# Kernel tuning notes

Hardware: AMD Instinct MI355X
Metric: run time of the kernel (lower is better)

Reference implementation:

```python
import jax, jax.numpy as jnp
import numpy as np

N_QUBITS = 14
LATENT = 14
DEPTH = 4
BATCH = 256
DIM = 1 << N_QUBITS  # 16384 amplitudes

# PennyLane convention: wire 0 is the most-significant bit of the flat state index.
_idx = np.arange(DIM)
_bits = (_idx[None, :] >> (N_QUBITS - 1 - np.arange(N_QUBITS)[:, None])) & 1  # [n_qubits, DIM]
_parity = np.sum(_bits[:-1] * _bits[1:], axis=0) % 2  # adjacent-pair CZ chain parity
CZ_SIGNS = jnp.asarray(1.0 - 2.0 * _parity, dtype=jnp.complex64)  # [DIM]
Z_SIGNS = jnp.asarray(1 - 2 * _bits[:LATENT], dtype=jnp.float32)  # [LATENT, DIM]


def _rx(t):
    c = jnp.cos(0.5 * t) + 0j
    s = -1j * jnp.sin(0.5 * t)
    m = jnp.stack([jnp.stack([c, s], -1), jnp.stack([s, c], -1)], -2)
    return m.astype(jnp.complex64)


def _ry(t):
    c = jnp.cos(0.5 * t)
    s = jnp.sin(0.5 * t)
    m = jnp.stack([jnp.stack([c, -s], -1), jnp.stack([s, c], -1)], -2)
    return m.astype(jnp.complex64)


def _rz(t):
    e = jnp.exp(-0.5j * t.astype(jnp.complex64))
    z = jnp.zeros_like(e)
    m = jnp.stack([jnp.stack([e, z], -1), jnp.stack([z, jnp.conj(e)], -1)], -2)
    return m.astype(jnp.complex64)


def _apply_1q(state, mat, wire):
    # state: [B, DIM]; mat: [2,2] (shared) or [B,2,2] (per-sample)
    B = state.shape[0]
    left = 1 << wire
    right = 1 << (N_QUBITS - wire - 1)
    st = state.reshape(B, left, 2, right)
    if mat.ndim == 3:
        st = jnp.einsum('bij,bajc->baic', mat, st)
    else:
        st = jnp.einsum('ij,bajc->baic', mat, st)
    return st.reshape(B, DIM)


def setup_inputs() -> dict:
    key = jax.random.key(0)
    k1, k2, k3, k4 = jax.random.split(key, 4)
    conditioning = jax.random.normal(k1, (BATCH, LATENT), dtype=jnp.float32)
    lim = 1.0 / np.sqrt(LATENT)
    W_enc = jax.random.uniform(k2, (N_QUBITS, LATENT), jnp.float32, -lim, lim)
    b_enc = jax.random.uniform(k3, (N_QUBITS,), jnp.float32, -lim, lim)
    # TorchLayer default init: U(0, 2*pi)
    weights = jax.random.uniform(k4, (DEPTH, N_QUBITS, 3), jnp.float32, 0.0, 2.0 * np.pi)
    return {"conditioning": conditioning, "W_enc": W_enc, "b_enc": b_enc, "weights": weights}


def reference(conditioning, W_enc, b_enc, weights):
    # encode: Linear + SiLU -> per-wire rotation angles [B, n_qubits]
    emb = conditioning @ W_enc.T + b_enc
    emb = emb * jax.nn.sigmoid(emb)
    B = emb.shape[0]

    state = jnp.zeros((B, DIM), jnp.complex64).at[:, 0].set(1.0)

    # angle encoding: RX(v) then RY(v) on each wire (per-sample gates)
    for w in range(N_QUBITS):
        v = emb[:, w]
        U = jnp.einsum('bij,bjk->bik', _ry(v), _rx(v))  # [B,2,2]
        state = _apply_1q(state, U, w)

    # variational layers: RZ, RX, RY per wire (shared gates), then CZ chain
    for d in range(DEPTH):
        for w in range(N_QUBITS):
            p = weights[d, w]
            U = _ry(p[2]) @ _rx(p[1]) @ _rz(p[0])  # [2,2]
            state = _apply_1q(state, U, w)
        state = state * CZ_SIGNS  # all adjacent CZs fused into one diagonal

    probs = state.real ** 2 + state.imag ** 2  # [B, DIM]
    latent = probs @ Z_SIGNS.T  # <Z_w> for w in range(LATENT) -> [B, LATENT]

    # F.layer_norm over last dim, no affine params
    mu = jnp.mean(latent, axis=-1, keepdims=True)
    var = jnp.var(latent, axis=-1, keepdims=True)
    return (latent - mu) / jnp.sqrt(var + 1e-5)
```

## Files before the change

### kernel.cpp

```cpp
#include <hip/hip_runtime.h>
#include <math.h>

#define NQ    14
#define DIM   16384
#define DEPTH 4

typedef __attribute__((ext_vector_type(2))) float f2;
typedef __attribute__((ext_vector_type(4))) float f4;

__device__ __forceinline__ f2 cmul(f2 a, f2 b) {
    return (f2){a.x*b.x - a.y*b.y, a.x*b.y + a.y*b.x};
}
__device__ __forceinline__ f2 cmac2(f2 x, f2 u, f2 us, f2 y, f2 v, f2 vs) {
    f2 r = x.xx * u;
    r += x.yy * us;
    r += y.xx * v;
    r += y.yy * vs;
    return r;
}


template<int CTRL>
__device__ __forceinline__ f2 dpp2(f2 v) {
    union U { f2 f; int i[2]; } u, r;
    u.f = v;
    r.i[0] = __builtin_amdgcn_update_dpp(0, u.i[0], CTRL, 0xF, 0xF, true);
    r.i[1] = __builtin_amdgcn_update_dpp(0, u.i[1], CTRL, 0xF, 0xF, true);
    return r.f;
}
template<int PAT>
__device__ __forceinline__ f2 swz2(f2 v) {
    union U { f2 f; int i[2]; } u, r;
    u.f = v;
    r.i[0] = __builtin_amdgcn_ds_swizzle(u.i[0], PAT);
    r.i[1] = __builtin_amdgcn_ds_swizzle(u.i[1], PAT);
    return r.f;
}
template<int XB> __device__ __forceinline__ f2 lxchg(f2 v);
template<> __device__ __forceinline__ f2 lxchg<1>(f2 v)  { return dpp2<0xB1>(v); }
template<> __device__ __forceinline__ f2 lxchg<2>(f2 v)  { return dpp2<0x4E>(v); }
template<> __device__ __forceinline__ f2 lxchg<4>(f2 v)  { return swz2<0x101F>(v); }
template<> __device__ __forceinline__ f2 lxchg<8>(f2 v)  { return dpp2<0x128>(v); }
template<> __device__ __forceinline__ f2 lxchg<16>(f2 v) { return swz2<0x401F>(v); }
template<> __device__ __forceinline__ f2 lxchg<32>(f2 v) {
    union U { f2 f; float s[2]; } u, r;
    u.f = v;
    r.s[0] = __shfl_xor(u.s[0], 32, 64);
    r.s[1] = __shfl_xor(u.s[1], 32, 64);
    return r.f;
}

template<int MASK>
__device__ __forceinline__ void reg_gate(f2 a[16], const f4* G) {
    f4 g0 = G[0], g1 = G[1], g2 = G[2], g3 = G[3];
    #pragma unroll
    for (int l = 0; l < 16; ++l) {
        if (l & MASK) continue;
        const int j = l | MASK;
        f2 x = a[l], y = a[j];
        a[l] = cmac2(x, g0.xy, g0.zw, y, g1.xy, g1.zw);
        a[j] = cmac2(x, g2.xy, g2.zw, y, g3.xy, g3.zw);
    }
}

template<int XB>
__device__ __forceinline__ void lane_gate(f2 a[16], const f4* G, int t) {
    const bool hi = (t & XB) != 0;
    f4 c1 = G[hi ? 3 : 0];
    f4 c2 = G[hi ? 2 : 1];
    #pragma unroll
    for (int l = 0; l < 16; ++l) {
        f2 p = lxchg<XB>(a[l]);
        a[l] = cmac2(a[l], c1.xy, c1.zw, p, c2.xy, c2.zw);
    }
}

__device__ __forceinline__ void cz_M0(f2 a[16], int t) {
    const int n = t & 63, w = t >> 6;
    const int pT = (__popc(w & (w >> 1)) + __popc(n & (n >> 1)) + ((n & 1) & (w >> 3))) & 1;
    const float F0 = pT ? -1.f : 1.f;
    const float F1 = (pT ^ ((n >> 5) & 1)) ? -1.f : 1.f;
    #pragma unroll
    for (int l = 0; l < 16; ++l) {
        float s = (l & 1) ? F1 : F0;
        if (__popc(l & (l >> 1)) & 1) s = -s;
        a[l] *= s;
    }
}

__device__ __forceinline__ void cz_M1(f2 a[16], int t) {
    const int n = t & 63, w = t >> 6;
    const int pT = (__popc(w & (w >> 1)) + __popc(n & (n >> 1)) + ((w & 1) & (n >> 5))) & 1;
    const float F0 = pT ? -1.f : 1.f;
    const float F1 = (pT ^ (n & 1)) ? -1.f : 1.f;
    #pragma unroll
    for (int l = 0; l < 16; ++l) {
        float s = (l & 8) ? F1 : F0;
        if (__popc(l & (l >> 1)) & 1) s = -s;
        a[l] *= s;
    }
}

__global__ __launch_bounds__(1024)
void qlg_kernel(const float* __restrict__ cond,
                const float* __restrict__ Wenc,
                const float* __restrict__ benc,
                const float* __restrict__ wts,
                float* __restrict__ out)
{
    __shared__ f2 st[DIM];
    __shared__ f4 gates[DEPTH][NQ][4];
    __shared__ f2 qv[NQ][2];
    __shared__ f2 Phi[128];
    __shared__ f2 Plo[128];
    __shared__ float embS[NQ];
    __shared__ float wred[16][NQ];
    __shared__ float lat[NQ];

    const int b = blockIdx.x;
    const int t = threadIdx.x;
    const int n = t & 63, w = t >> 6;
    const int bM1 = n | (w << 10);

    if (t < NQ) {
        float s = benc[t];
        #pragma unroll
        for (int k = 0; k < NQ; ++k) s += cond[b*NQ + k] * Wenc[t*NQ + k];
        embS[t] = s / (1.0f + __expf(-s));
    }
    if (t >= 64 && t < 64 + DEPTH*NQ) {
        const int gi = t - 64;
        const int d = gi / NQ, ww = gi % NQ;
        const float p0 = wts[(d*NQ + ww)*3 + 0];
        const float p1 = wts[(d*NQ + ww)*3 + 1];
        const float p2 = wts[(d*NQ + ww)*3 + 2];
        float s0, c0, s1, c1, s2, c2;
        sincosf(0.5f*p0, &s0, &c0);
        sincosf(0.5f*p1, &s1, &c1);
        sincosf(0.5f*p2, &s2, &c2);
        f2 e0  = (f2){c0, -s0};
        f2 e0c = (f2){c0,  s0};
        f2 is1 = (f2){0.f, -s1};
        f2 m00 = c1 * e0;
        f2 m01 = cmul(is1, e0c);
        f2 m10 = cmul(is1, e0);
        f2 m11 = c1 * e0c;
        f2 u00 = c2*m00 - s2*m10;
        f2 u01 = c2*m01 - s2*m11;
        f2 u10 = s2*m00 + c2*m10;
        f2 u11 = s2*m01 + c2*m11;
        gates[d][ww][0] = (f4){u00.x, u00.y, -u00.y, u00.x};
        gates[d][ww][1] = (f4){u01.x, u01.y, -u01.y, u01.x};
        gates[d][ww][2] = (f4){u10.x, u10.y, -u10.y, u10.x};
        gates[d][ww][3] = (f4){u11.x, u11.y, -u11.y, u11.x};
    }
    __syncthreads();

    if (t < NQ) {
        float v = embS[t];
        float s, c;
        sincosf(0.5f*v, &s, &c);
        f2 a0 = (f2){c*c,  s*s};
        f2 a1 = (f2){s*c, -s*c};
        f2 u00 = gates[0][t][0].xy, u01 = gates[0][t][1].xy;
        f2 u10 = gates[0][t][2].xy, u11 = gates[0][t][3].xy;
        qv[t][0] = cmul(u00, a0) + cmul(u01, a1);
        qv[t][1] = cmul(u10, a0) + cmul(u11, a1);
    }
    __syncthreads();

    if (t < 128) {
        f2 p = qv[0][(t >> 6) & 1];
        #pragma unroll
        for (int ww = 1; ww <= 6; ++ww) p = cmul(p, qv[ww][(t >> (6 - ww)) & 1]);
        Phi[t] = p;
    } else if (t < 256) {
        const int j = t - 128;
        f2 p = qv[7][(j >> 6) & 1];
        #pragma unroll
        for (int ww = 8; ww <= 13; ++ww) p = cmul(p, qv[ww][(j >> (13 - ww)) & 1]);
        Plo[j] = p;
    }
    __syncthreads();

    f2 a[16];
    {
        f2 plo = Plo[((n & 7) << 4) | w];
        #pragma unroll
        for (int l = 0; l < 16; ++l)
            a[l] = cmul(Phi[(l << 3) | (n >> 3)], plo);
        cz_M0(a, t);
    }

    {
        const f4 (*gl)[4] = gates[1];
        reg_gate<8>(a, gl[0]);
        reg_gate<4>(a, gl[1]);
        reg_gate<2>(a, gl[2]);
        reg_gate<1>(a, gl[3]);
        lane_gate<32>(a, gl[4], t);
        lane_gate<16>(a, gl[5], t);
        lane_gate<8>(a, gl[6], t);
        lane_gate<4>(a, gl[7], t);
        lane_gate<2>(a, gl[8], t);
        lane_gate<1>(a, gl[9], t);
    }

    #pragma unroll
    for (int l = 0; l < 16; ++l) st[t + (l << 10)] = a[l];
    __syncthreads();
    #pragma unroll
    for (int l = 0; l < 16; ++l) a[l] = st[bM1 + (l << 6)];

    {
        const f4 (*gl1)[4] = gates[1];
        reg_gate<8>(a, gl1[10]);
        reg_gate<4>(a, gl1[11]);
        reg_gate<2>(a, gl1[12]);
        reg_gate<1>(a, gl1[13]);
        cz_M1(a, t);
        const f4 (*gl2)[4] = gates[2];
        lane_gate<32>(a, gl2[4], t);
        lane_gate<16>(a, gl2[5], t);
        lane_gate<8>(a, gl2[6], t);
        lane_gate<4>(a, gl2[7], t);
        lane_gate<2>(a, gl2[8], t);
        lane_gate<1>(a, gl2[9], t);
        reg_gate<8>(a, gl2[10]);
        reg_gate<4>(a, gl2[11]);
        reg_gate<2>(a, gl2[12]);
        reg_gate<1>(a, gl2[13]);
    }

    __syncthreads();
    #pragma unroll
    for (int l = 0; l < 16; ++l) st[bM1 + (l << 6)] = a[l];
    __syncthreads();
    #pragma unroll
    for (int l = 0; l < 16; ++l) a[l] = st[t + (l << 10)];

    {
        const f4 (*gl2)[4] = gates[2];
        reg_gate<8>(a, gl2[0]);
        reg_gate<4>(a, gl2[1]);
        reg_gate<2>(a, gl2[2]);
        reg_gate<1>(a, gl2[3]);
        cz_M0(a, t);
        const f4 (*gl3)[4] = gates[3];
        reg_gate<8>(a, gl3[0]);
        reg_gate<4>(a, gl3[1]);
        reg_gate<2>(a, gl3[2]);
        reg_gate<1>(a, gl3[3]);
        lane_gate<32>(a, gl3[4], t);
        lane_gate<16>(a, gl3[5], t);
        lane_gate<8>(a, gl3[6], t);
        lane_gate<4>(a, gl3[7], t);
        lane_gate<2>(a, gl3[8], t);
        lane_gate<1>(a, gl3[9], t);
    }

    __syncthreads();
    #pragma unroll
    for (int l = 0; l < 16; ++l) st[t + (l << 10)] = a[l];
    __syncthreads();
    #pragma unroll
    for (int l = 0; l < 16; ++l) a[l] = st[bM1 + (l << 6)];

    float SU, Q10, Q11, Q12, Q13;
    {
        const f4 (*gl3)[4] = gates[3];
        reg_gate<8>(a, gl3[10]);
        reg_gate<4>(a, gl3[11]);
        reg_gate<2>(a, gl3[12]);
        reg_gate<1>(a, gl3[13]);
        SU = Q10 = Q11 = Q12 = Q13 = 0.f;
        #pragma unroll
        for (int l = 0; l < 16; ++l) {
            float p = a[l].x*a[l].x + a[l].y*a[l].y;
            SU  += p;
            Q10 += (l & 8) ? -p : p;
            Q11 += (l & 4) ? -p : p;
            Q12 += (l & 2) ? -p : p;
            Q13 += (l & 1) ? -p : p;
        }
    }

    {
        const int lane = t & 63, wv = t >> 6;
        #pragma unroll
        for (int ww = 0; ww < NQ; ++ww) {
            float v;
            if      (ww == 10) v = Q10;
            else if (ww == 11) v = Q11;
            else if (ww == 12) v = Q12;
            else if (ww == 13) v = Q13;
            else               v = ((t >> (9 - ww)) & 1) ? -SU : SU;
            #pragma unroll
            for (int off = 32; off > 0; off >>= 1) v += __shfl_down(v, off, 64);
            if (lane == 0) wred[wv][ww] = v;
        }
    }
    __syncthreads();
    if (t < NQ) {
        float s = 0.f;
        #pragma unroll
        for (int k = 0; k < 16; ++k) s += wred[k][t];
        lat[t] = s;
    }
    __syncthreads();
    if (t < NQ) {
        float mu = 0.f;
        #pragma unroll
        for (int k = 0; k < NQ; ++k) mu += lat[k];
        mu *= (1.0f / NQ);
        float var = 0.f;
        #pragma unroll
        for (int k = 0; k < NQ; ++k) { float dv = lat[k] - mu; var += dv*dv; }
        var *= (1.0f / NQ);
        out[b*NQ + t] = (lat[t] - mu) * rsqrtf(var + 1e-5f);
    }
}

extern "C" void kernel_launch(void* const* d_in, const int* in_sizes, int n_in,
                              void* d_out, int out_size, void* d_ws, size_t ws_size,
                              hipStream_t stream)
{
    (void)n_in; (void)d_ws; (void)ws_size; (void)out_size;
    const float* cond = (const float*)d_in[0];
    const float* Wenc = (const float*)d_in[1];
    const float* benc = (const float*)d_in[2];
    const float* wts  = (const float*)d_in[3];
    float* out = (float*)d_out;
    const int B = in_sizes[0] / NQ;
    qlg_kernel<<<dim3(B), dim3(1024), 0, stream>>>(cond, Wenc, benc, wts, out);
}
```

Baseline: 95.81 us.

## Remap qubit-to-lane layout so all lane gates use DPP, dropping swizzle and shuffles

Changes how qubits map to lanes and registers in the two state layouts. Lane-resident qubits now sit only on lane bits 1, 2 and 8, which DPP can reach, so the ds_swizzle and shfl_xor exchanges for lane bits 4, 16 and 32 are no longer needed. Gates are regrouped across the shared-memory transposes to fit the new mapping. CZ parity and Z-sign bit extraction are rewritten for the permuted layout. The aim is to cut cross-lane exchange cost, at the risk of subtle correctness errors in the permutation.

```diff
diff --git a/kernel.cpp b/kernel.cpp
--- a/kernel.cpp
+++ b/kernel.cpp
@@ -28,27 +28,10 @@
     r.i[1] = __builtin_amdgcn_update_dpp(0, u.i[1], CTRL, 0xF, 0xF, true);
     return r.f;
 }
-template<int PAT>
-__device__ __forceinline__ f2 swz2(f2 v) {
-    union U { f2 f; int i[2]; } u, r;
-    u.f = v;
-    r.i[0] = __builtin_amdgcn_ds_swizzle(u.i[0], PAT);
-    r.i[1] = __builtin_amdgcn_ds_swizzle(u.i[1], PAT);
-    return r.f;
-}
 template<int XB> __device__ __forceinline__ f2 lxchg(f2 v);
-template<> __device__ __forceinline__ f2 lxchg<1>(f2 v)  { return dpp2<0xB1>(v); }
-template<> __device__ __forceinline__ f2 lxchg<2>(f2 v)  { return dpp2<0x4E>(v); }
-template<> __device__ __forceinline__ f2 lxchg<4>(f2 v)  { return swz2<0x101F>(v); }
-template<> __device__ __forceinline__ f2 lxchg<8>(f2 v)  { return dpp2<0x128>(v); }
-template<> __device__ __forceinline__ f2 lxchg<16>(f2 v) { return swz2<0x401F>(v); }
-template<> __device__ __forceinline__ f2 lxchg<32>(f2 v) {
-    union U { f2 f; float s[2]; } u, r;
-    u.f = v;
-    r.s[0] = __shfl_xor(u.s[0], 32, 64);
-    r.s[1] = __shfl_xor(u.s[1], 32, 64);
-    return r.f;
-}
+template<> __device__ __forceinline__ f2 lxchg<1>(f2 v) { return dpp2<0xB1>(v); }
+template<> __device__ __forceinline__ f2 lxchg<2>(f2 v) { return dpp2<0x4E>(v); }
+template<> __device__ __forceinline__ f2 lxchg<8>(f2 v) { return dpp2<0x128>(v); }
 
 template<int MASK>
 __device__ __forceinline__ void reg_gate(f2 a[16], const f4* G) {
@@ -75,7 +58,7 @@
     }
 }
 
-__device__ __forceinline__ void cz_M0(f2 a[16], int t) {
+__device__ __forceinline__ void cz_A(f2 a[16], int t) {
     const int n = t & 63, w = t >> 6;
     const int pT = (__popc(w & (w >> 1)) + __popc(n & (n >> 1)) + ((n & 1) & (w >> 3))) & 1;
     const float F0 = pT ? -1.f : 1.f;
@@ -88,11 +71,14 @@
     }
 }
 
-__device__ __forceinline__ void cz_M1(f2 a[16], int t) {
+__device__ __forceinline__ void cz_B(f2 a[16], int t) {
     const int n = t & 63, w = t >> 6;
-    const int pT = (__popc(w & (w >> 1)) + __popc(n & (n >> 1)) + ((w & 1) & (n >> 5))) & 1;
+    const int n0 = n & 1, n1 = (n >> 1) & 1, n2 = (n >> 2) & 1;
+    const int n3 = (n >> 3) & 1, n4 = (n >> 4) & 1, n5 = (n >> 5) & 1;
+    const int pT = ((n2 & n4) ^ (n4 & n0) ^ (n0 & n5) ^ (n5 & n1) ^ (n1 & n3)
+                    ^ (n3 & (w & 1)) ^ (__popc(w & (w >> 1)) & 1));
     const float F0 = pT ? -1.f : 1.f;
-    const float F1 = (pT ^ (n & 1)) ? -1.f : 1.f;
+    const float F1 = (pT ^ n2) ? -1.f : 1.f;
     #pragma unroll
     for (int l = 0; l < 16; ++l) {
         float s = (l & 8) ? F1 : F0;
@@ -120,7 +106,10 @@
     const int b = blockIdx.x;
     const int t = threadIdx.x;
     const int n = t & 63, w = t >> 6;
-    const int bM1 = n | (w << 10);
+    const int bB = (w << 10)
+                 | (((n >> 3) & 1) << 5) | (((n >> 1) & 1) << 4)
+                 | (((n >> 5) & 1) << 3) | ((n & 1) << 2)
+                 | (((n >> 4) & 1) << 1) | ((n >> 2) & 1);
 
     if (t < NQ) {
         float s = benc[t];
@@ -189,7 +178,7 @@
         #pragma unroll
         for (int l = 0; l < 16; ++l)
             a[l] = cmul(Phi[(l << 3) | (n >> 3)], plo);
-        cz_M0(a, t);
+        cz_A(a, t);
     }
 
     {
@@ -198,10 +187,7 @@
         reg_gate<4>(a, gl[1]);
         reg_gate<2>(a, gl[2]);
         reg_gate<1>(a, gl[3]);
-        lane_gate<32>(a, gl[4], t);
-        lane_gate<16>(a, gl[5], t);
         lane_gate<8>(a, gl[6], t);
-        lane_gate<4>(a, gl[7], t);
         lane_gate<2>(a, gl[8], t);
         lane_gate<1>(a, gl[9], t);
     }
@@ -210,7 +196,7 @@
     for (int l = 0; l < 16; ++l) st[t + (l << 10)] = a[l];
     __syncthreads();
     #pragma unroll
-    for (int l = 0; l < 16; ++l) a[l] = st[bM1 + (l << 6)];
+    for (int l = 0; l < 16; ++l) a[l] = st[bB + (l << 6)];
 
     {
         const f4 (*gl1)[4] = gates[1];
@@ -218,23 +204,23 @@
         reg_gate<4>(a, gl1[11]);
         reg_gate<2>(a, gl1[12]);
         reg_gate<1>(a, gl1[13]);
-        cz_M1(a, t);
+        lane_gate<8>(a, gl1[4], t);
+        lane_gate<2>(a, gl1[5], t);
+        lane_gate<1>(a, gl1[7], t);
+        cz_B(a, t);
         const f4 (*gl2)[4] = gates[2];
-        lane_gate<32>(a, gl2[4], t);
-        lane_gate<16>(a, gl2[5], t);
-        lane_gate<8>(a, gl2[6], t);
-        lane_gate<4>(a, gl2[7], t);
-        lane_gate<2>(a, gl2[8], t);
-        lane_gate<1>(a, gl2[9], t);
         reg_gate<8>(a, gl2[10]);
         reg_gate<4>(a, gl2[11]);
         reg_gate<2>(a, gl2[12]);
         reg_gate<1>(a, gl2[13]);
-    }
-
-    __syncthreads();
-    #pragma unroll
-    for (int l = 0; l < 16; ++l) st[bM1 + (l << 6)] = a[l];
+        lane_gate<8>(a, gl2[4], t);
+        lane_gate<2>(a, gl2[5], t);
+        lane_gate<1>(a, gl2[7], t);
+    }
+
+    __syncthreads();
+    #pragma unroll
+    for (int l = 0; l < 16; ++l) st[bB + (l << 6)] = a[l];
     __syncthreads();
     #pragma unroll
     for (int l = 0; l < 16; ++l) a[l] = st[t + (l << 10)];
@@ -245,16 +231,16 @@
         reg_gate<4>(a, gl2[1]);
         reg_gate<2>(a, gl2[2]);
         reg_gate<1>(a, gl2[3]);
-        cz_M0(a, t);
+        lane_gate<8>(a, gl2[6], t);
+        lane_gate<2>(a, gl2[8], t);
+        lane_gate<1>(a, gl2[9], t);
+        cz_A(a, t);
         const f4 (*gl3)[4] = gates[3];
         reg_gate<8>(a, gl3[0]);
         reg_gate<4>(a, gl3[1]);
         reg_gate<2>(a, gl3[2]);
         reg_gate<1>(a, gl3[3]);
-        lane_gate<32>(a, gl3[4], t);
-        lane_gate<16>(a, gl3[5], t);
         lane_gate<8>(a, gl3[6], t);
-        lane_gate<4>(a, gl3[7], t);
         lane_gate<2>(a, gl3[8], t);
         lane_gate<1>(a, gl3[9], t);
     }
@@ -264,7 +250,7 @@
     for (int l = 0; l < 16; ++l) st[t + (l << 10)] = a[l];
     __syncthreads();
     #pragma unroll
-    for (int l = 0; l < 16; ++l) a[l] = st[bM1 + (l << 6)];
+    for (int l = 0; l < 16; ++l) a[l] = st[bB + (l << 6)];
 
     float SU, Q10, Q11, Q12, Q13;
     {
@@ -273,6 +259,9 @@
         reg_gate<4>(a, gl3[11]);
         reg_gate<2>(a, gl3[12]);
         reg_gate<1>(a, gl3[13]);
+        lane_gate<8>(a, gl3[4], t);
+        lane_gate<2>(a, gl3[5], t);
+        lane_gate<1>(a, gl3[7], t);
         SU = Q10 = Q11 = Q12 = Q13 = 0.f;
         #pragma unroll
         for (int l = 0; l < 16; ++l) {
@@ -287,6 +276,7 @@
 
     {
         const int lane = t & 63, wv = t >> 6;
+        const int sbit[10] = {9, 8, 7, 6, 3, 1, 5, 0, 4, 2};
         #pragma unroll
         for (int ww = 0; ww < NQ; ++ww) {
             float v;
@@ -294,7 +284,7 @@
             else if (ww == 11) v = Q11;
             else if (ww == 12) v = Q12;
             else if (ww == 13) v = Q13;
-            else               v = ((t >> (9 - ww)) & 1) ? -SU : SU;
+            else               v = ((t >> sbit[ww]) & 1) ? -SU : SU;
             #pragma unroll
             for (int off = 32; off > 0; off >>= 1) v += __shfl_down(v, off, 64);
             if (lane == 0) wred[wv][ww] = v;
```

Measured after the change: 95.15 us. No clear change (-0.7%).
